# Performance work log

Hardware: AMD Instinct MI355X
Metric: run time of the kernel (lower is better)

The kernel has to match this reference:

```python
import jax, jax.numpy as jnp
import numpy as np

# SMPL kinematic tree (parents[0] is the root and unused in the loop)
PARENTS = (0, 0, 0, 0, 1, 2, 3, 4, 5, 6, 7, 8, 9, 9, 9, 12, 13, 14, 16, 17, 18, 19, 20, 21)
N_BATCH, N_VERTS, N_JOINTS, N_BETAS, N_POSE, N_COCO = 1024, 6890, 24, 10, 207, 19


def setup_inputs() -> dict:
    key = jax.random.key(0)
    ks = jax.random.split(key, 8)
    return {
        "beta": jax.random.normal(ks[0], (N_BATCH, N_BETAS), jnp.float32) * 0.5,
        "theta": jax.random.normal(ks[1], (N_BATCH, N_JOINTS * 3), jnp.float32) * 0.3,
        "v_template": jax.random.normal(ks[2], (N_VERTS, 3), jnp.float32),
        "shapedirs": jax.random.normal(ks[3], (N_BETAS, N_VERTS * 3), jnp.float32) * 0.01,
        "J_regressor": jax.random.uniform(ks[4], (N_VERTS, N_JOINTS), jnp.float32) / N_VERTS,
        "posedirs": jax.random.normal(ks[5], (N_POSE, N_VERTS * 3), jnp.float32) * 0.01,
        "weights": jax.random.uniform(ks[6], (N_VERTS, N_JOINTS), jnp.float32),
        "joint_regressor": jax.random.uniform(ks[7], (N_VERTS, N_COCO), jnp.float32) / N_VERTS,
    }


def batch_rodrigues(theta):
    """theta: (M, 3) axis-angle -> (M, 3, 3) rotation matrices."""
    angle = jnp.sqrt(jnp.sum(theta * theta, axis=-1, keepdims=True) + 1e-8)  # (M,1)
    r = theta / angle
    c = jnp.cos(angle)[..., None]  # (M,1,1)
    s = jnp.sin(angle)[..., None]
    rx, ry, rz = r[:, 0], r[:, 1], r[:, 2]
    z = jnp.zeros_like(rx)
    K = jnp.stack([z, -rz, ry, rz, z, -rx, -ry, rx, z], axis=-1).reshape(-1, 3, 3)
    outer = r[:, :, None] * r[:, None, :]
    eye = jnp.eye(3, dtype=theta.dtype)
    return c * eye + s * K + (1.0 - c) * outer


def global_rigid_transform(Rs, J):
    """Rs: (N,24,3,3), J: (N,24,3) -> (J_transformed (N,24,3), A (N,24,4,4))."""
    N = Rs.shape[0]
    bot = jnp.broadcast_to(jnp.array([0.0, 0.0, 0.0, 1.0], Rs.dtype), (N, 1, 4))

    def make_A(R, t):  # R: (N,3,3), t: (N,3)
        top = jnp.concatenate([R, t[:, :, None]], axis=2)  # (N,3,4)
        return jnp.concatenate([top, bot], axis=1)  # (N,4,4)

    results = [make_A(Rs[:, 0], J[:, 0])]
    for i in range(1, N_JOINTS):
        t_rel = J[:, i] - J[:, PARENTS[i]]
        results.append(jnp.matmul(results[PARENTS[i]], make_A(Rs[:, i], t_rel)))
    res = jnp.stack(results, axis=1)  # (N,24,4,4)
    J_transformed = res[:, :, :3, 3]
    # A = res - pack(res @ [J; 0]) : subtract rotated rest joints from translation column
    J_homo = jnp.concatenate([J, jnp.zeros((N, N_JOINTS, 1), Rs.dtype)], axis=2)  # (N,24,4)
    init_bone = jnp.einsum('njab,njb->nja', res, J_homo)  # (N,24,4)
    A = res - jnp.concatenate([jnp.zeros((N, N_JOINTS, 4, 3), Rs.dtype), init_bone[..., None]], axis=-1)
    return J_transformed, A


def reference(beta, theta, v_template, shapedirs, J_regressor, posedirs, weights, joint_regressor):
    N = beta.shape[0]
    # shape blend: (N,10) @ (10, V*3) -> (N,V,3)
    v_shaped = (beta @ shapedirs).reshape(N, N_VERTS, 3) + v_template
    # rest-pose joints: (N,V,3) x (V,24) -> (N,24,3)
    J = jnp.einsum('nva,vj->nja', v_shaped, J_regressor)
    # pose rotations
    Rs = batch_rodrigues(theta.reshape(-1, 3)).reshape(N, N_JOINTS, 3, 3)
    # pose blend: (N,207) @ (207, V*3)
    pose_feature = (Rs[:, 1:] - jnp.eye(3, dtype=Rs.dtype)).reshape(N, N_POSE)
    v_posed = (pose_feature @ posedirs).reshape(N, N_VERTS, 3) + v_shaped
    # kinematic chain
    _, A = global_rigid_transform(Rs, J)
    # LBS: per-vertex 4x4 transform
    T = jnp.einsum('vj,njab->nvab', weights, A)  # (N,V,4,4)
    v_homo = jnp.concatenate([v_posed, jnp.ones((N, N_VERTS, 1), v_posed.dtype)], axis=2)
    verts = jnp.einsum('nvab,nvb->nva', T, v_homo)[:, :, :3]  # (N,V,3)
    joints = jnp.einsum('nva,vj->nja', verts, joint_regressor)  # (N,19,3)
    return joints
```

## Files before the change

kernel.cpp:

```cpp
#include <hip/hip_runtime.h>

#define NB 1024
#define NV 6890
#define VP 6912
#define NJ 24
#define NBETA 10
#define NPOSE 207
#define NK 19
#define NKJ 456
#define NCOL 1368
#define KR 218
#define AR 219
#define VSTR 20670
#define RTP 16
#define NVC 216
#define CFP 32
#define KSPLIT 27
#define KSTEPS 8

typedef __attribute__((ext_vector_type(8))) short bf16x8;
typedef __attribute__((ext_vector_type(4))) float f32x4;

#define AP_PLANE ((size_t)3*RTP*NVC*64*8)
#define BP_PLANE ((size_t)CFP*NVC*64*8)
#define USH_TOTAL (2*AP_PLANE + 2*BP_PLANE)
#define SZ_OUT   ((size_t)AR*NCOL)
#define SZ_COEF  ((size_t)KR*NB)
#define SZ_AW    ((size_t)NB*288)
#define SZ_JS    (11ull*24*3)
#define SZ_M     ((size_t)NB*NCOL)

__device__ inline void bf_split(float x, unsigned short& h, unsigned short& l) {
    unsigned u = __float_as_uint(x);
    h = (unsigned short)(u >> 16);
    float hf = __uint_as_float((unsigned)h << 16);
    float lf = x - hf;
    l = (unsigned short)(__float_as_uint(lf) >> 16);
}

__global__ __launch_bounds__(256) void k_at2(const float* __restrict__ pd,
                                             const float* __restrict__ sd,
                                             const float* __restrict__ vt,
                                             unsigned short* __restrict__ APH,
                                             unsigned short* __restrict__ APL) {
    int tid = threadIdx.x;
    int u = blockIdx.x * 4 + (tid >> 6);
    int rt = u / NVC, vc = u - rt * NVC;
    int rl = tid & 15, lh = (tid >> 4) & 3;
    int r = rt * 16 + rl;
    int v0 = (vc * 4 + lh) * 8;

    float f[24];
    if (r >= AR) {
#pragma unroll
        for (int i = 0; i < 24; i++) f[i] = 0.f;
    } else if (r == 218) {
#pragma unroll
        for (int i = 0; i < 24; i++) f[i] = (v0 + i / 3 < NV) ? 1.0f : 0.f;
    } else {
        const float* src = (r < NPOSE) ? (pd + (size_t)r * VSTR)
                         : (r < 217)   ? (sd + (size_t)(r - NPOSE) * VSTR)
                                       : vt;
        if (v0 + 8 <= NV) {
            const float2* p = (const float2*)(src + 3 * v0);
#pragma unroll
            for (int q = 0; q < 12; q++) {
                float2 t = p[q];
                f[2 * q] = t.x; f[2 * q + 1] = t.y;
            }
        } else {
#pragma unroll
            for (int i = 0; i < 24; i++)
                f[i] = (v0 + i / 3 < NV) ? src[3 * v0 + i] : 0.f;
        }
    }

    int lane = lh * 16 + rl;
#pragma unroll
    for (int a = 0; a < 3; a++) {
        union { unsigned short u16[8]; int4 v4; } H, L;
#pragma unroll
        for (int e = 0; e < 8; e++) bf_split(f[3 * e + a], H.u16[e], L.u16[e]);
        size_t off = (((size_t)(a * RTP + rt) * NVC + vc) * 64 + lane) * 8;
        *(int4*)&APH[off] = H.v4;
        *(int4*)&APL[off] = L.v4;
    }
}

__global__ __launch_bounds__(256) void k_cw2(const float* __restrict__ jr,
                                             const float* __restrict__ w,
                                             unsigned short* __restrict__ BPH,
                                             unsigned short* __restrict__ BPL) {
    int tid = threadIdx.x;
    int u = blockIdx.x * 4 + (tid >> 6);
    int cf = u / NVC, vc = u - cf * NVC;
    int cl = tid & 15, lh = (tid >> 4) & 3;
    int col = cf * 16 + cl;
    int v0 = (vc * 4 + lh) * 8;
    int k = col / NJ, j = col - k * NJ;
    bool okc = (col < NKJ);

    union { unsigned short u16[8]; int4 v4; } H, L;
#pragma unroll
    for (int e = 0; e < 8; e++) {
        int v = v0 + e;
        float val = (okc && v < NV) ? jr[v * NK + k] * w[v * NJ + j] : 0.f;
        bf_split(val, H.u16[e], L.u16[e]);
    }
    size_t off = (((size_t)cf * NVC + vc) * 64 + (lh * 16 + cl)) * 8;
    *(int4*)&BPH[off] = H.v4;
    *(int4*)&BPL[off] = L.v4;
}

__global__ __launch_bounds__(256) void k_js2(const float* __restrict__ Jreg,
                                             const float* __restrict__ sd,
                                             const float* __restrict__ vt,
                                             float* __restrict__ JS) {
    int row = blockIdx.x % 11;
    int c   = blockIdx.x / 11;
    int tid = threadIdx.x;
    int lane = tid & 63;
    const float* src = (row < NBETA) ? (sd + (size_t)row * VSTR) : vt;

    float acc[72];
#pragma unroll
    for (int o = 0; o < 72; o++) acc[o] = 0.f;

    for (int iv = 0; iv < 4; ++iv) {
        int v = c * 1024 + iv * 256 + tid;
        float jrg[24];
        float s0 = 0.f, s1 = 0.f, s2 = 0.f;
        if (v < NV) {
#pragma unroll
            for (int q = 0; q < 6; q++) {
                float4 f = *(const float4*)&Jreg[v * NJ + q * 4];
                jrg[q * 4 + 0] = f.x; jrg[q * 4 + 1] = f.y;
                jrg[q * 4 + 2] = f.z; jrg[q * 4 + 3] = f.w;
            }
            s0 = src[3 * v]; s1 = src[3 * v + 1]; s2 = src[3 * v + 2];
        } else {
#pragma unroll
            for (int q = 0; q < 24; q++) jrg[q] = 0.f;
        }
#pragma unroll
        for (int j = 0; j < 24; j++) {
            acc[j * 3 + 0] += jrg[j] * s0;
            acc[j * 3 + 1] += jrg[j] * s1;
            acc[j * 3 + 2] += jrg[j] * s2;
        }
    }
#pragma unroll
    for (int o = 0; o < 72; o++) {
#pragma unroll
        for (int off = 1; off < 64; off <<= 1)
            acc[o] += __shfl_xor(acc[o], off);
    }
    if (lane == 0) {
#pragma unroll
        for (int o = 0; o < 72; o++) atomicAdd(&JS[row * 72 + o], acc[o]);
    }
}

__global__ __launch_bounds__(64) void k_pose(const float* __restrict__ beta,
                                             const float* __restrict__ theta,
                                             const float* __restrict__ JS,
                                             float* __restrict__ coefT,
                                             float* __restrict__ Aw) {
    int n = blockIdx.x;
    int tid = threadIdx.x;
    __shared__ float Rs[24][9];
    __shared__ float Jl[24][3];
    __shared__ float G[24][12];

    if (tid < NJ) {
        int j = tid;
        float x = theta[n * 72 + j * 3 + 0];
        float y = theta[n * 72 + j * 3 + 1];
        float z = theta[n * 72 + j * 3 + 2];
        float ang = sqrtf(x * x + y * y + z * z + 1e-8f);
        float inv = 1.0f / ang;
        float rx = x * inv, ry = y * inv, rz = z * inv;
        float ct = cosf(ang), st = sinf(ang), oc = 1.0f - ct;
        float R[9];
        R[0] = ct + oc * rx * rx;  R[1] = -st * rz + oc * rx * ry; R[2] =  st * ry + oc * rx * rz;
        R[3] =  st * rz + oc * ry * rx; R[4] = ct + oc * ry * ry;  R[5] = -st * rx + oc * ry * rz;
        R[6] = -st * ry + oc * rz * rx; R[7] =  st * rx + oc * rz * ry; R[8] = ct + oc * rz * rz;
#pragma unroll
        for (int e = 0; e < 9; e++) Rs[j][e] = R[e];
        if (j >= 1) {
#pragma unroll
            for (int e = 0; e < 9; e++)
                coefT[(size_t)((j - 1) * 9 + e) * NB + n] =
                    R[e] - ((e == 0 || e == 4 || e == 8) ? 1.0f : 0.0f);
        }
    }
    if (tid < NBETA) coefT[(size_t)(NPOSE + tid) * NB + n] = beta[n * NBETA + tid];
    if (tid == 63)   coefT[(size_t)217 * NB + n] = 1.0f;
    __syncthreads();

    for (int idx = tid; idx < 72; idx += 64) {
        int j = idx / 3, a = idx - j * 3;
        float acc = JS[(NBETA * NJ + j) * 3 + a];
#pragma unroll
        for (int b = 0; b < NBETA; b++) acc += beta[n * NBETA + b] * JS[(b * NJ + j) * 3 + a];
        Jl[j][a] = acc;
    }
    __syncthreads();

    if (tid < 12) {
        int r = tid >> 2, cc = tid & 3;
        G[0][tid] = (cc < 3) ? Rs[0][r * 3 + cc] : Jl[0][r];
    }
    __syncthreads();

    const int PAR[24] = {0,0,0,0,1,2,3,4,5,6,7,8,9,9,9,12,13,14,16,17,18,19,20,21};
#pragma unroll
    for (int i = 1; i < NJ; i++) {
        int p = PAR[i];
        if (tid < 12) {
            int r = tid >> 2, cc = tid & 3;
            float g0 = G[p][r * 4 + 0], g1 = G[p][r * 4 + 1];
            float g2 = G[p][r * 4 + 2], g3 = G[p][r * 4 + 3];
            float val;
            if (cc < 3) {
                val = g0 * Rs[i][cc] + g1 * Rs[i][3 + cc] + g2 * Rs[i][6 + cc];
            } else {
                float t0 = Jl[i][0] - Jl[p][0];
                float t1 = Jl[i][1] - Jl[p][1];
                float t2 = Jl[i][2] - Jl[p][2];
                val = g0 * t0 + g1 * t1 + g2 * t2 + g3;
            }
            G[i][tid] = val;
        }
        __syncthreads();
    }

    for (int idx = tid; idx < 288; idx += 64) {
        int j = idx / 12, e = idx - j * 12;
        float val;
        if (e < 9) {
            int r = e / 3, cc = e - 3 * (e / 3);
            val = G[j][r * 4 + cc];
        } else {
            int r = e - 9;
            val = G[j][r * 4 + 3] -
                  (G[j][r * 4 + 0] * Jl[j][0] + G[j][r * 4 + 1] * Jl[j][1] +
                   G[j][r * 4 + 2] * Jl[j][2]);
        }
        Aw[(size_t)n * 288 + idx] = val;
    }
}

#define LOADF(S, AH, AL, BH, BL) do {                                   \
    int _o = (S) * 512;                                                  \
    _Pragma("unroll") for (int mi = 0; mi < 4; mi++) {                   \
        AH[mi] = *(const bf16x8*)(APH + oA[mi] + _o);                    \
        AL[mi] = *(const bf16x8*)(APL + oA[mi] + _o); }                  \
    _Pragma("unroll") for (int ni = 0; ni < 2; ni++) {                   \
        BH[ni] = *(const bf16x8*)(BPH + oB[ni] + _o);                    \
        BL[ni] = *(const bf16x8*)(BPL + oB[ni] + _o); }                  \
} while (0)

#define MFMAF(AH, AL, BH, BL) do {                                       \
    _Pragma("unroll") for (int mi = 0; mi < 4; mi++)                     \
    _Pragma("unroll") for (int ni = 0; ni < 2; ni++) {                   \
        acc[mi][ni] = __builtin_amdgcn_mfma_f32_16x16x32_bf16(AH[mi], BH[ni], acc[mi][ni], 0, 0, 0); \
        acc[mi][ni] = __builtin_amdgcn_mfma_f32_16x16x32_bf16(AH[mi], BL[ni], acc[mi][ni], 0, 0, 0); \
        acc[mi][ni] = __builtin_amdgcn_mfma_f32_16x16x32_bf16(AL[mi], BH[ni], acc[mi][ni], 0, 0, 0); } \
} while (0)

__global__ __launch_bounds__(256) void k_gemmP(const unsigned short* __restrict__ APH,
                                               const unsigned short* __restrict__ APL,
                                               const unsigned short* __restrict__ BPH,
                                               const unsigned short* __restrict__ BPL,
                                               float* __restrict__ OUTB) {
    int bid = blockIdx.x;
    int logical = (bid & 7) * 162 + (bid >> 3);
    int ks = logical / 48;
    int rem = logical - ks * 48;
    int a  = rem >> 4;
    int mt = (rem >> 3) & 1;
    int nt = rem & 7;

    int tid = threadIdx.x;
    int lane = tid & 63, wv = tid >> 6;
    int wm = wv >> 1, wn = wv & 1;
    int lr = lane & 15, lc = lane >> 4;

    int vc0 = ks * KSTEPS;
    int oA[4], oB[2];
#pragma unroll
    for (int mi = 0; mi < 4; mi++)
        oA[mi] = (((a * RTP + mt * 8 + wm * 4 + mi) * NVC + vc0) * 64 + lane) * 8;
#pragma unroll
    for (int ni = 0; ni < 2; ni++)
        oB[ni] = (((nt * 4 + wn * 2 + ni) * NVC + vc0) * 64 + lane) * 8;

    f32x4 acc[4][2] = {};
    bf16x8 aH0[4], aL0[4], bH0[2], bL0[2];
    bf16x8 aH1[4], aL1[4], bH1[2], bL1[2];

    LOADF(0, aH0, aL0, bH0, bL0);
#pragma unroll
    for (int s = 0; s < KSTEPS; ++s) {
        if ((s & 1) == 0) {
            if (s + 1 < KSTEPS) LOADF(s + 1, aH1, aL1, bH1, bL1);
            MFMAF(aH0, aL0, bH0, bL0);
        } else {
            if (s + 1 < KSTEPS) LOADF(s + 1, aH0, aL0, bH0, bL0);
            MFMAF(aH1, aL1, bH1, bL1);
        }
    }

#pragma unroll
    for (int mi = 0; mi < 4; mi++) {
        int r0 = mt * 128 + wm * 64 + mi * 16 + lc * 4;
        if (r0 >= AR) continue;
#pragma unroll
        for (int ni = 0; ni < 2; ni++) {
            int c = nt * 64 + wn * 32 + ni * 16 + lr;
            if (c >= NKJ) continue;
#pragma unroll
            for (int q = 0; q < 4; ++q) {
                int r = r0 + q;
                if (r < AR)
                    atomicAdd(&OUTB[(size_t)r * NCOL + a * NKJ + c], acc[mi][ni][q]);
            }
        }
    }
}

__global__ __launch_bounds__(256) void k_gemmM(const float* __restrict__ coefT,
                                               const float* __restrict__ OUTB,
                                               float* __restrict__ M) {
    int bid = blockIdx.x;
    int mt = bid & 31, nt = bid >> 5;
    int mb = mt * 32, nb = nt * 64;
    __shared__ float Cs[2][32][32];
    __shared__ float Bs[2][32][64];
    int tid = threadIdx.x;
    int tm = tid & 15, tn = tid >> 4;

    float rc[4], rb[8];
#define LOADM(T) do {                                                    \
    int _kb = (T) * 32;                                                  \
    _Pragma("unroll") for (int p = 0; p < 4; p++) {                      \
        int idx = tid + p * 256;                                         \
        int kk = idx >> 5, nl = idx & 31;                                \
        int r = _kb + kk;                                                \
        rc[p] = (r < KR) ? coefT[(size_t)r * NB + mb + nl] : 0.f; }      \
    _Pragma("unroll") for (int p = 0; p < 8; p++) {                      \
        int idx = tid + p * 256;                                         \
        int kk = idx >> 6, m = idx & 63;                                 \
        int r = _kb + kk;                                                \
        int col = nb + m;                                                \
        rb[p] = (r < KR && col < NCOL) ? OUTB[(size_t)r * NCOL + col] : 0.f; } \
} while (0)

    LOADM(0);
    float acc[2][4] = {};
    int cur = 0;
    for (int t = 0; t < 7; ++t) {
#pragma unroll
        for (int p = 0; p < 4; p++) {
            int idx = tid + p * 256;
            Cs[cur][idx >> 5][idx & 31] = rc[p];
        }
#pragma unroll
        for (int p = 0; p < 8; p++) {
            int idx = tid + p * 256;
            Bs[cur][idx >> 6][idx & 63] = rb[p];
        }
        __syncthreads();
        if (t < 6) LOADM(t + 1);
#pragma unroll
        for (int kk = 0; kk < 32; kk++) {
            float2 cv = *(const float2*)&Cs[cur][kk][tm * 2];
            float4 bv = *(const float4*)&Bs[cur][kk][tn * 4];
            float cm[2] = {cv.x, cv.y};
            float bn[4] = {bv.x, bv.y, bv.z, bv.w};
#pragma unroll
            for (int i = 0; i < 2; i++)
#pragma unroll
                for (int j = 0; j < 4; j++) acc[i][j] += cm[i] * bn[j];
        }
        __syncthreads();
        cur ^= 1;
    }
#pragma unroll
    for (int i = 0; i < 2; i++) {
        int n = mb + tm * 2 + i;
#pragma unroll
        for (int j = 0; j < 4; j++) {
            int col = nb + tn * 4 + j;
            if (col < NCOL) M[(size_t)n * NCOL + col] = acc[i][j];
        }
    }
}

__global__ void k_joints(const float* __restrict__ M, const float* __restrict__ Aw,
                         const float* __restrict__ OUTB, float* __restrict__ out) {
    int idx = blockIdx.x * 256 + threadIdx.x;
    if (idx >= NB * NK * 3) return;
    int n = idx / (NK * 3);
    int rem = idx - n * (NK * 3);
    int k = rem / 3, a = rem - k * 3;
    const float* A = Aw + (size_t)n * 288;
    const float* Mn = M + (size_t)n * NCOL;
    float o = 0.f;
#pragma unroll
    for (int j = 0; j < NJ; j++) {
        int kj = k * NJ + j;
        const float* Aj = A + j * 12;
        o += Aj[a * 3 + 0] * Mn[kj]
           + Aj[a * 3 + 1] * Mn[NKJ + kj]
           + Aj[a * 3 + 2] * Mn[2 * NKJ + kj]
           + OUTB[(size_t)218 * NCOL + kj] * Aj[9 + a];
    }
    out[idx] = o;
}

extern "C" void kernel_launch(void* const* d_in, const int* in_sizes, int n_in,
                              void* d_out, int out_size, void* d_ws, size_t ws_size,
                              hipStream_t stream) {
    const float* beta  = (const float*)d_in[0];
    const float* theta = (const float*)d_in[1];
    const float* vt    = (const float*)d_in[2];
    const float* sd    = (const float*)d_in[3];
    const float* Jreg  = (const float*)d_in[4];
    const float* pd    = (const float*)d_in[5];
    const float* w     = (const float*)d_in[6];
    const float* jr    = (const float*)d_in[7];

    unsigned short* ush = (unsigned short*)d_ws;
    unsigned short* APH = ush;
    unsigned short* APL = APH + AP_PLANE;
    unsigned short* BPH = APL + AP_PLANE;
    unsigned short* BPL = BPH + BP_PLANE;
    float* fbase = (float*)(ush + USH_TOTAL);
    float* OUTB  = fbase;
    float* coefT = OUTB + SZ_OUT;
    float* Aw    = coefT + SZ_COEF;
    float* JS    = Aw + SZ_AW;
    float* M     = JS + SZ_JS;
    float* out   = (float*)d_out;

    hipMemsetAsync(OUTB, 0, (SZ_OUT + SZ_COEF + SZ_AW + SZ_JS) * sizeof(float), stream);
    k_at2<<<16 * NVC / 4, 256, 0, stream>>>(pd, sd, vt, APH, APL);
    k_cw2<<<CFP * NVC / 4, 256, 0, stream>>>(jr, w, BPH, BPL);
    k_js2<<<11 * 7, 256, 0, stream>>>(Jreg, sd, vt, JS);
    k_pose<<<NB, 64, 0, stream>>>(beta, theta, JS, coefT, Aw);
    k_gemmP<<<2 * 8 * 3 * KSPLIT, 256, 0, stream>>>(APH, APL, BPH, BPL, OUTB);
    k_gemmM<<<32 * 22, 256, 0, stream>>>(coefT, OUTB, M);
    k_joints<<<(NB * NK * 3 + 255) / 256, 256, 0, stream>>>(M, Aw, OUTB, out);
}
```

Measured before the change: 209.1 us.

## Stage GEMM tiles through LDS with async global-to-LDS loads and reduce K-split

Result: faster. 186.9 us (-10.6%).

```diff
diff --git a/kernel.cpp b/kernel.cpp
--- a/kernel.cpp
+++ b/kernel.cpp
@@ -15,8 +15,8 @@
 #define RTP 16
 #define NVC 216
 #define CFP 32
-#define KSPLIT 27
-#define KSTEPS 8
+#define KSPLIT 12
+#define KSTEPS 18
 
 typedef __attribute__((ext_vector_type(8))) short bf16x8;
 typedef __attribute__((ext_vector_type(4))) float f32x4;
@@ -251,31 +251,13 @@
     }
 }
 
-#define LOADF(S, AH, AL, BH, BL) do {                                   \
-    int _o = (S) * 512;                                                  \
-    _Pragma("unroll") for (int mi = 0; mi < 4; mi++) {                   \
-        AH[mi] = *(const bf16x8*)(APH + oA[mi] + _o);                    \
-        AL[mi] = *(const bf16x8*)(APL + oA[mi] + _o); }                  \
-    _Pragma("unroll") for (int ni = 0; ni < 2; ni++) {                   \
-        BH[ni] = *(const bf16x8*)(BPH + oB[ni] + _o);                    \
-        BL[ni] = *(const bf16x8*)(BPL + oB[ni] + _o); }                  \
-} while (0)
-
-#define MFMAF(AH, AL, BH, BL) do {                                       \
-    _Pragma("unroll") for (int mi = 0; mi < 4; mi++)                     \
-    _Pragma("unroll") for (int ni = 0; ni < 2; ni++) {                   \
-        acc[mi][ni] = __builtin_amdgcn_mfma_f32_16x16x32_bf16(AH[mi], BH[ni], acc[mi][ni], 0, 0, 0); \
-        acc[mi][ni] = __builtin_amdgcn_mfma_f32_16x16x32_bf16(AH[mi], BL[ni], acc[mi][ni], 0, 0, 0); \
-        acc[mi][ni] = __builtin_amdgcn_mfma_f32_16x16x32_bf16(AL[mi], BH[ni], acc[mi][ni], 0, 0, 0); } \
-} while (0)
-
 __global__ __launch_bounds__(256) void k_gemmP(const unsigned short* __restrict__ APH,
                                                const unsigned short* __restrict__ APL,
                                                const unsigned short* __restrict__ BPH,
                                                const unsigned short* __restrict__ BPL,
                                                float* __restrict__ OUTB) {
     int bid = blockIdx.x;
-    int logical = (bid & 7) * 162 + (bid >> 3);
+    int logical = (bid & 7) * 72 + (bid >> 3);
     int ks = logical / 48;
     int rem = logical - ks * 48;
     int a  = rem >> 4;
@@ -287,29 +269,65 @@
     int wm = wv >> 1, wn = wv & 1;
     int lr = lane & 15, lc = lane >> 4;
 
+    int aBase = a * RTP + mt * 8;
+    int nBase = nt * 4;
+
+    __shared__ __align__(16) unsigned short stage[2][24 * 512];
+
+#define STAGE(B, VC) do {                                                        \
+    _Pragma("unroll")                                                            \
+    for (int q = 0; q < 6; ++q) {                                                \
+        int f = wv * 6 + q;                                                      \
+        const unsigned short* g;                                                 \
+        if (f < 16) {                                                            \
+            int rt_l = f >> 1;                                                   \
+            const unsigned short* pl = (f & 1) ? APL : APH;                      \
+            g = pl + (((size_t)(aBase + rt_l) * NVC + (VC)) << 9) + lane * 8;    \
+        } else {                                                                 \
+            int cf_l = (f - 16) >> 1;                                            \
+            const unsigned short* pl = (f & 1) ? BPL : BPH;                      \
+            g = pl + (((size_t)(nBase + cf_l) * NVC + (VC)) << 9) + lane * 8;    \
+        }                                                                        \
+        __builtin_amdgcn_global_load_lds(                                        \
+            (const __attribute__((address_space(1))) unsigned int*)g,            \
+            (__attribute__((address_space(3))) unsigned int*)&stage[B][f * 512], \
+            16, 0, 0);                                                           \
+    }                                                                            \
+} while (0)
+
+    f32x4 acc[4][2] = {};
     int vc0 = ks * KSTEPS;
-    int oA[4], oB[2];
-#pragma unroll
-    for (int mi = 0; mi < 4; mi++)
-        oA[mi] = (((a * RTP + mt * 8 + wm * 4 + mi) * NVC + vc0) * 64 + lane) * 8;
-#pragma unroll
-    for (int ni = 0; ni < 2; ni++)
-        oB[ni] = (((nt * 4 + wn * 2 + ni) * NVC + vc0) * 64 + lane) * 8;
-
-    f32x4 acc[4][2] = {};
-    bf16x8 aH0[4], aL0[4], bH0[2], bL0[2];
-    bf16x8 aH1[4], aL1[4], bH1[2], bL1[2];
-
-    LOADF(0, aH0, aL0, bH0, bL0);
-#pragma unroll
-    for (int s = 0; s < KSTEPS; ++s) {
-        if ((s & 1) == 0) {
-            if (s + 1 < KSTEPS) LOADF(s + 1, aH1, aL1, bH1, bL1);
-            MFMAF(aH0, aL0, bH0, bL0);
-        } else {
-            if (s + 1 < KSTEPS) LOADF(s + 1, aH0, aL0, bH0, bL0);
-            MFMAF(aH1, aL1, bH1, bL1);
-        }
+
+    STAGE(0, vc0);
+    __syncthreads();
+
+    int cur = 0;
+    for (int t = 0; t < KSTEPS; ++t) {
+        if (t + 1 < KSTEPS) STAGE(cur ^ 1, vc0 + t + 1);
+
+        bf16x8 aH[4], aL[4], bH[2], bL[2];
+#pragma unroll
+        for (int mi = 0; mi < 4; mi++) {
+            int rt_l = wm * 4 + mi;
+            aH[mi] = *(const bf16x8*)&stage[cur][(2 * rt_l) * 512 + lane * 8];
+            aL[mi] = *(const bf16x8*)&stage[cur][(2 * rt_l + 1) * 512 + lane * 8];
+        }
+#pragma unroll
+        for (int ni = 0; ni < 2; ni++) {
+            int cf_l = wn * 2 + ni;
+            bH[ni] = *(const bf16x8*)&stage[cur][(16 + 2 * cf_l) * 512 + lane * 8];
+            bL[ni] = *(const bf16x8*)&stage[cur][(16 + 2 * cf_l + 1) * 512 + lane * 8];
+        }
+#pragma unroll
+        for (int mi = 0; mi < 4; mi++)
+#pragma unroll
+            for (int ni = 0; ni < 2; ni++) {
+                acc[mi][ni] = __builtin_amdgcn_mfma_f32_16x16x32_bf16(aH[mi], bH[ni], acc[mi][ni], 0, 0, 0);
+                acc[mi][ni] = __builtin_amdgcn_mfma_f32_16x16x32_bf16(aH[mi], bL[ni], acc[mi][ni], 0, 0, 0);
+                acc[mi][ni] = __builtin_amdgcn_mfma_f32_16x16x32_bf16(aL[mi], bH[ni], acc[mi][ni], 0, 0, 0);
+            }
+        __syncthreads();
+        cur ^= 1;
     }
 
 #pragma unroll
```
